# Kernel optimization log

Measured on AMD Instinct MI355X. Metric: run time of the kernel, lower is better.

## Reference

```python
import jax, jax.numpy as jnp
import numpy as np

Q_DIM = 1024
K_DIM = 1024
EMBED_DIM = 1024
NUM_HEADS = 16
HEAD_DIM = EMBED_DIM // NUM_HEADS
CLAMP = 50000.0
MASK_FILL = -9000000000000000.0


def _xavier(key, out_f, in_f):
    bound = float(np.sqrt(6.0 / (in_f + out_f)))
    return jax.random.uniform(key, (out_f, in_f), jnp.float32, -bound, bound)


def setup_inputs() -> dict:
    key = jax.random.key(0)
    ks = jax.random.split(key, 8)
    b, t, s = 2, 2048, 2048
    return {
        "q": jax.random.normal(ks[0], (b, t, Q_DIM), jnp.float32),
        "k": jax.random.normal(ks[1], (b, s, K_DIM), jnp.float32),
        "v": jax.random.normal(ks[2], (b, s, K_DIM), jnp.float32),
        "attention_mask": jax.random.randint(ks[3], (b, s), 0, 2, jnp.int32),
        "Wq": _xavier(ks[4], EMBED_DIM, Q_DIM), "bq": jnp.zeros((EMBED_DIM,), jnp.float32),
        "Wk": _xavier(ks[5], EMBED_DIM, K_DIM), "bk": jnp.zeros((EMBED_DIM,), jnp.float32),
        "Wv": _xavier(ks[6], EMBED_DIM, K_DIM), "bv": jnp.zeros((EMBED_DIM,), jnp.float32),
        "Wo": _xavier(ks[7], Q_DIM, EMBED_DIM), "bo": jnp.zeros((Q_DIM,), jnp.float32),
    }


def reference(q, k, v, attention_mask, Wq, bq, Wk, bk, Wv, bv, Wo, bo):
    b, t, _ = q.shape
    s = k.shape[1]
    scale = HEAD_DIM ** (-0.5)
    # projections, split heads: [b, h, len, d]
    qs = ((q @ Wq.T + bq) * scale).reshape(b, t, NUM_HEADS, HEAD_DIM).transpose(0, 2, 1, 3)
    ks = (k @ Wk.T + bk).reshape(b, s, NUM_HEADS, HEAD_DIM).transpose(0, 2, 1, 3)
    vs = (v @ Wv.T + bv).reshape(b, s, NUM_HEADS, HEAD_DIM).transpose(0, 2, 1, 3)
    # scores [b, h, t, s], clamp for under/overflow as in original
    attn = jnp.einsum("bhtd,bhsd->bhts", qs, ks)
    attn = jnp.clip(attn, -CLAMP, CLAMP)
    # 2D mask -> additive: zeros become -9e15, nonzeros are ADDED as-is (faithful to masked_fill semantics)
    m = attention_mask.astype(jnp.float32)
    m = jnp.where(m == 0, MASK_FILL, m)  # [b, s]
    attn = attn + m[:, None, None, :]
    attn = jax.nn.softmax(attn, axis=-1)
    # dropout p=0 / eval mode: identity
    out = jnp.einsum("bhts,bhsd->bthd", attn, vs).reshape(b, t, EMBED_DIM)
    out = out @ Wo.T + bo
    return out, attn.reshape(b * NUM_HEADS, t, s)
```

## Files before the change

kernel.cpp:

```cpp
#include <hip/hip_runtime.h>
#include <hip/hip_bf16.h>


typedef __attribute__((ext_vector_type(8))) __bf16 bf16x8;
typedef __attribute__((ext_vector_type(4))) float f32x4;
typedef __attribute__((ext_vector_type(8))) unsigned short us8;

#define MFMA16(A, B, C) __builtin_amdgcn_mfma_f32_16x16x32_bf16(A, B, C, 0, 0, 0)

__device__ __forceinline__ unsigned short f2bf(float f) {
  __bf16 h = (__bf16)f;
  return __builtin_bit_cast(unsigned short, h);
}

__global__ __launch_bounds__(256) void cvt_all_kernel(
    const float* __restrict__ q, const float* __restrict__ k, const float* __restrict__ v,
    const float* __restrict__ Wq, const float* __restrict__ Wk,
    const float* __restrict__ Wv, const float* __restrict__ Wo,
    unsigned short* __restrict__ qb, unsigned short* __restrict__ kb,
    unsigned short* __restrict__ vb, unsigned short* __restrict__ wqb,
    unsigned short* __restrict__ wkb, unsigned short* __restrict__ wvb,
    unsigned short* __restrict__ wob) {
  const int bid = blockIdx.x;
  const float* src;
  unsigned short* dst;
  int i;
  if (bid < 4096)       { src = q; dst = qb; i = bid * 256 + threadIdx.x; }
  else if (bid < 8192)  { src = k; dst = kb; i = (bid - 4096) * 256 + threadIdx.x; }
  else if (bid < 12288) { src = v; dst = vb; i = (bid - 8192) * 256 + threadIdx.x; }
  else {
    int wsel = (bid - 12288) >> 10;
    i = ((bid - 12288) & 1023) * 256 + threadIdx.x;
    src = wsel == 0 ? Wq : wsel == 1 ? Wk : wsel == 2 ? Wv : Wo;
    dst = wsel == 0 ? wqb : wsel == 1 ? wkb : wsel == 2 ? wvb : wob;
  }
  float4 vv = ((const float4*)src)[i];
  ushort4 o;
  o.x = f2bf(vv.x); o.y = f2bf(vv.y); o.z = f2bf(vv.z); o.w = f2bf(vv.w);
  ((ushort4*)dst)[i] = o;
}

template <bool OUT_F32>
__device__ __forceinline__ void gemm_body(
    const unsigned short* __restrict__ A, const unsigned short* __restrict__ Bw,
    const float* __restrict__ bias, void* __restrict__ Cout, float scale,
    int m0, int n0) {
  __shared__ short As[128 * 72];
  __shared__ short Bs[128 * 72];
  const int tid = threadIdx.x;
  const int l = tid & 63, w = tid >> 6;
  const int lq = l >> 4, lr = l & 15;
  const int wr = w >> 1, wc = w & 1;

  uint4 va[4], vb[4];
#pragma unroll
  for (int i = 0; i < 4; ++i) {
    int c = i * 256 + tid, r = c >> 3, c8 = c & 7;
    va[i] = *(const uint4*)(A + (size_t)(m0 + r) * 1024 + c8 * 8);
    vb[i] = *(const uint4*)(Bw + (size_t)(n0 + r) * 1024 + c8 * 8);
  }
  const f32x4 fz = {0.f, 0.f, 0.f, 0.f};
  f32x4 acc[4][4];
#pragma unroll
  for (int m = 0; m < 4; ++m)
#pragma unroll
    for (int n = 0; n < 4; ++n) acc[m][n] = fz;

  for (int ks = 0; ks < 16; ++ks) {
    __syncthreads();
#pragma unroll
    for (int i = 0; i < 4; ++i) {
      int c = i * 256 + tid, r = c >> 3, c8 = c & 7;
      *(uint4*)((char*)As + r * 144 + c8 * 16) = va[i];
      *(uint4*)((char*)Bs + r * 144 + c8 * 16) = vb[i];
    }
    __syncthreads();
    if (ks < 15) {
      int k0 = (ks + 1) * 64;
#pragma unroll
      for (int i = 0; i < 4; ++i) {
        int c = i * 256 + tid, r = c >> 3, c8 = c & 7;
        va[i] = *(const uint4*)(A + (size_t)(m0 + r) * 1024 + k0 + c8 * 8);
        vb[i] = *(const uint4*)(Bw + (size_t)(n0 + r) * 1024 + k0 + c8 * 8);
      }
    }
#pragma unroll
    for (int kk = 0; kk < 2; ++kk) {
      bf16x8 af[4], bfr[4];
#pragma unroll
      for (int m = 0; m < 4; ++m)
        af[m] = *(const bf16x8*)((const char*)As + (wr * 64 + m * 16 + lr) * 144 + kk * 64 + lq * 16);
#pragma unroll
      for (int n = 0; n < 4; ++n)
        bfr[n] = *(const bf16x8*)((const char*)Bs + (wc * 64 + n * 16 + lr) * 144 + kk * 64 + lq * 16);
#pragma unroll
      for (int m = 0; m < 4; ++m)
#pragma unroll
        for (int n = 0; n < 4; ++n) acc[m][n] = MFMA16(af[m], bfr[n], acc[m][n]);
    }
  }
#pragma unroll
  for (int n = 0; n < 4; ++n) {
    const int col = n0 + wc * 64 + n * 16 + lr;
    const float bv_ = bias[col];
#pragma unroll
    for (int m = 0; m < 4; ++m) {
      const int rowb = m0 + wr * 64 + m * 16 + lq * 4;
#pragma unroll
      for (int r = 0; r < 4; ++r) {
        float vv = (acc[m][n][r] + bv_) * scale;
        if (OUT_F32)
          ((float*)Cout)[(size_t)(rowb + r) * 1024 + col] = vv;
        else
          ((unsigned short*)Cout)[(size_t)(rowb + r) * 1024 + col] = f2bf(vv);
      }
    }
  }
}

__global__ __launch_bounds__(256) void gemm_qkv_kernel(
    const unsigned short* __restrict__ qb, const unsigned short* __restrict__ kb,
    const unsigned short* __restrict__ vb,
    const unsigned short* __restrict__ wqb, const unsigned short* __restrict__ wkb,
    const unsigned short* __restrict__ wvb,
    const float* __restrict__ bq, const float* __restrict__ bk, const float* __restrict__ bv,
    unsigned short* __restrict__ Qp, unsigned short* __restrict__ Kp,
    unsigned short* __restrict__ Vp) {
  const int z = blockIdx.z;
  const unsigned short* A = z == 0 ? qb : z == 1 ? kb : vb;
  const unsigned short* W = z == 0 ? wqb : z == 1 ? wkb : wvb;
  const float* bias = z == 0 ? bq : z == 1 ? bk : bv;
  unsigned short* C = z == 0 ? Qp : z == 1 ? Kp : Vp;
  const float scale = z == 0 ? 0.125f : 1.0f;
  gemm_body<false>(A, W, bias, C, scale, blockIdx.x * 128, blockIdx.y * 128);
}

__global__ __launch_bounds__(256) void gemm_o_kernel(
    const unsigned short* __restrict__ A, const unsigned short* __restrict__ Bw,
    const float* __restrict__ bias, float* __restrict__ Cout) {
  gemm_body<true>(A, Bw, bias, Cout, 1.0f, blockIdx.x * 128, blockIdx.y * 128);
}

__global__ __launch_bounds__(256) void transpose_v_kernel(const unsigned short* __restrict__ Vp,
                                                          unsigned short* __restrict__ Vt) {
  __shared__ unsigned short Ts[64 * 72];
  const int tid = threadIdx.x;
  const int kt = blockIdx.x;
  const int rt = blockIdx.y;
  const int b_ = rt >> 4, h_ = rt & 15;
#pragma unroll
  for (int i = 0; i < 2; ++i) {
    int c = i * 256 + tid, r = c >> 3, c8 = c & 7;
    uint4 v = *(const uint4*)(Vp + (size_t)(b_ * 2048 + kt * 64 + r) * 1024 + h_ * 64 + c8 * 8);
    *(uint4*)((char*)Ts + r * 144 + c8 * 16) = v;
  }
  __syncthreads();
#pragma unroll
  for (int i = 0; i < 2; ++i) {
    int c = i * 256 + tid, dr = c >> 3, k8 = c & 7;
    us8 t8;
#pragma unroll
    for (int j = 0; j < 8; ++j) t8[j] = Ts[(k8 * 8 + j) * 72 + dr];
    *(us8*)(Vt + (size_t)(rt * 64 + dr) * 2048 + kt * 64 + k8 * 8) = t8;
  }
}

__device__ __forceinline__ int pf_idx(int row, int col) {
  return row * 64 + (((col >> 2) ^ (row & 7)) << 2) + (col & 3);
}

__global__ __launch_bounds__(256) void attn_kernel(
    const unsigned short* __restrict__ Qp,
    const unsigned short* __restrict__ Kp,
    const unsigned short* __restrict__ Vt,
    const int* __restrict__ mask,
    float* __restrict__ attn_out,
    unsigned short* __restrict__ Obuf)
{
  __shared__ char smem[61440];
  short* Qs = (short*)smem;
  float* maskadd = (float*)(smem + 53248);

  const int tid = threadIdx.x;
  const int l = tid & 63, w = tid >> 6;
  const int lq = l >> 4, lr = l & 15;
  float* Pw = (float*)(smem + w * 4096);

  const int tb = blockIdx.x, h = blockIdx.y, bz = blockIdx.z;
  const size_t qrow0 = (size_t)bz * 2048 + tb * 64;
  const size_t krow0 = (size_t)bz * 2048;
  const size_t vrow0 = (size_t)(bz * 16 + h) * 64;

  for (int j = tid; j < 2048; j += 256) {
    int mv = mask[bz * 2048 + j];
    maskadd[j] = (mv == 0) ? -9.0e15f : (float)mv;
  }
#pragma unroll
  for (int i = 0; i < 2; ++i) {
    int c = i * 256 + tid, r = c >> 3, c8 = c & 7;
    uint4 v = *(const uint4*)(Qp + (qrow0 + r) * 1024 + h * 64 + c8 * 8);
    *(uint4*)((char*)Qs + r * 144 + c8 * 16) = v;
  }
  __syncthreads();
  bf16x8 aq[2];
#pragma unroll
  for (int kk = 0; kk < 2; ++kk)
    aq[kk] = *(const bf16x8*)((const char*)Qs + (w * 16 + lr) * 144 + kk * 64 + lq * 16);
  __syncthreads();

  const int r0 = tid >> 3, c8s = tid & 7;

#define KLOAD(d, kcv)                                                                       \
  {                                                                                         \
    d[0] = *(const uint4*)(Kp + (krow0 + (kcv)*64 + r0) * 1024 + h * 64 + c8s * 8);         \
    d[1] = *(const uint4*)(Kp + (krow0 + (kcv)*64 + 32 + r0) * 1024 + h * 64 + c8s * 8);    \
  }
#define VLOAD(d, kcv)                                                                       \
  {                                                                                         \
    d[0] = *(const uint4*)(Vt + (vrow0 + r0) * 2048 + (kcv)*64 + c8s * 8);                  \
    d[1] = *(const uint4*)(Vt + (vrow0 + 32 + r0) * 2048 + (kcv)*64 + c8s * 8);             \
  }
#define KWRITE(s, buf)                                                          \
  {                                                                             \
    *(uint4*)(smem + 16384 + (buf)*9216 + r0 * 144 + c8s * 16) = s[0];          \
    *(uint4*)(smem + 16384 + (buf)*9216 + (32 + r0) * 144 + c8s * 16) = s[1];   \
  }
#define VWRITE(s, buf)                                                          \
  {                                                                             \
    *(uint4*)(smem + 34816 + (buf)*9216 + r0 * 144 + c8s * 16) = s[0];          \
    *(uint4*)(smem + 34816 + (buf)*9216 + (32 + r0) * 144 + c8s * 16) = s[1];   \
  }
#define KFRAG(jt, kk) \
  (*(const bf16x8*)(smem + 16384 + (kc & 1) * 9216 + ((jt)*16 + lr) * 144 + (kk)*64 + lq * 16))
#define VFRAG(dt, kk) \
  (*(const bf16x8*)(smem + 34816 + (kc & 1) * 9216 + ((dt)*16 + lr) * 144 + (kk)*64 + lq * 16))

  float lacc[4] = {0.f, 0.f, 0.f, 0.f};
  {
    uint4 kr[2];
    KLOAD(kr, 0);
    KWRITE(kr, 0);
    __syncthreads();
    for (int kc = 0; kc < 32; ++kc) {
      uint4 kn[2];
      if (kc < 31) KLOAD(kn, kc + 1);
#pragma unroll
      for (int jt = 0; jt < 4; ++jt) {
        f32x4 sa = {0.f, 0.f, 0.f, 0.f};
        sa = MFMA16(aq[0], KFRAG(jt, 0), sa);
        sa = MFMA16(aq[1], KFRAG(jt, 1), sa);
        float ma = maskadd[kc * 64 + jt * 16 + lr];
#pragma unroll
        for (int r = 0; r < 4; ++r) {
          float s_ = fminf(fmaxf(sa[r], -50000.f), 50000.f) + ma;
          lacc[r] += __expf(s_);
        }
      }
      if (kc < 31) KWRITE(kn, (kc + 1) & 1);
      __syncthreads();
    }
  }
#pragma unroll
  for (int r = 0; r < 4; ++r) {
    float t = lacc[r];
    t += __shfl_xor(t, 1, 64);
    t += __shfl_xor(t, 2, 64);
    t += __shfl_xor(t, 4, 64);
    t += __shfl_xor(t, 8, 64);
    lacc[r] = 1.0f / t;
  }

  const f32x4 fz = {0.f, 0.f, 0.f, 0.f};
  f32x4 oacc[4];
#pragma unroll
  for (int dt = 0; dt < 4; ++dt) oacc[dt] = fz;
  const size_t arow = (size_t)(bz * 16 + h) * 2048 + tb * 64 + w * 16;

  {
    uint4 kr[2], vr[2];
    KLOAD(kr, 0);
    VLOAD(vr, 0);
    KWRITE(kr, 0);
    VWRITE(vr, 0);
    __syncthreads();
    for (int kc = 0; kc < 32; ++kc) {
      uint4 kn[2], vn[2];
      if (kc < 31) {
        KLOAD(kn, kc + 1);
        VLOAD(vn, kc + 1);
      }
#pragma unroll
      for (int jt = 0; jt < 4; ++jt) {
        f32x4 sa = {0.f, 0.f, 0.f, 0.f};
        sa = MFMA16(aq[0], KFRAG(jt, 0), sa);
        sa = MFMA16(aq[1], KFRAG(jt, 1), sa);
        float ma = maskadd[kc * 64 + jt * 16 + lr];
#pragma unroll
        for (int r = 0; r < 4; ++r) {
          float s_ = fminf(fmaxf(sa[r], -50000.f), 50000.f) + ma;
          Pw[pf_idx(lq * 4 + r, jt * 16 + lr)] = __expf(s_) * lacc[r];
        }
      }
#pragma unroll
      for (int it = 0; it < 4; ++it) {
        int row = it * 4 + lq;
        f32x4 pv4 = *(const f32x4*)&Pw[pf_idx(row, lr * 4)];
        f32x4* dst = (f32x4*)&attn_out[(arow + row) * 2048 + kc * 64 + lr * 4];
        __builtin_nontemporal_store(pv4, dst);
      }
#pragma unroll
      for (int kk = 0; kk < 2; ++kk) {
        f32x4 a0 = *(const f32x4*)&Pw[pf_idx(lr, kk * 32 + lq * 8)];
        f32x4 a1 = *(const f32x4*)&Pw[pf_idx(lr, kk * 32 + lq * 8 + 4)];
        bf16x8 ap;
#pragma unroll
        for (int j = 0; j < 4; ++j) {
          ap[j] = (__bf16)a0[j];
          ap[4 + j] = (__bf16)a1[j];
        }
#pragma unroll
        for (int dt = 0; dt < 4; ++dt)
          oacc[dt] = MFMA16(ap, VFRAG(dt, kk), oacc[dt]);
      }
      if (kc < 31) {
        KWRITE(kn, (kc + 1) & 1);
        VWRITE(vn, (kc + 1) & 1);
      }
      __syncthreads();
    }
  }
#pragma unroll
  for (int dt = 0; dt < 4; ++dt) {
    int col = h * 64 + dt * 16 + lr;
#pragma unroll
    for (int r = 0; r < 4; ++r) {
      int trow = tb * 64 + w * 16 + lq * 4 + r;
      Obuf[((size_t)bz * 2048 + trow) * 1024 + col] = f2bf(oacc[dt][r]);
    }
  }
#undef KLOAD
#undef VLOAD
#undef KWRITE
#undef VWRITE
#undef KFRAG
#undef VFRAG
}

extern "C" void kernel_launch(void* const* d_in, const int* in_sizes, int n_in,
                              void* d_out, int out_size, void* d_ws, size_t ws_size,
                              hipStream_t stream) {
  (void)in_sizes; (void)n_in; (void)out_size; (void)ws_size;
  const float* q  = (const float*)d_in[0];
  const float* k  = (const float*)d_in[1];
  const float* v  = (const float*)d_in[2];
  const int* msk  = (const int*)d_in[3];
  const float* Wq = (const float*)d_in[4];
  const float* bq = (const float*)d_in[5];
  const float* Wk = (const float*)d_in[6];
  const float* bk = (const float*)d_in[7];
  const float* Wv = (const float*)d_in[8];
  const float* bv = (const float*)d_in[9];
  const float* Wo = (const float*)d_in[10];
  const float* bo = (const float*)d_in[11];

  unsigned short* p = (unsigned short*)d_ws;
  unsigned short* qb  = p; p += 4194304;
  unsigned short* kb  = p; p += 4194304;
  unsigned short* vb  = p; p += 4194304;
  unsigned short* wqb = p; p += 1048576;
  unsigned short* wkb = p; p += 1048576;
  unsigned short* wvb = p; p += 1048576;
  unsigned short* wob = p; p += 1048576;
  unsigned short* Qp  = p; p += 4194304;
  unsigned short* Kp  = p; p += 4194304;
  unsigned short* Vp  = p; p += 4194304;
  unsigned short* Vtg = p; p += 4194304;
  unsigned short* Ob  = p; p += 4194304;

  cvt_all_kernel<<<16384, 256, 0, stream>>>(q, k, v, Wq, Wk, Wv, Wo,
                                            qb, kb, vb, wqb, wkb, wvb, wob);

  gemm_qkv_kernel<<<dim3(32, 8, 3), 256, 0, stream>>>(qb, kb, vb, wqb, wkb, wvb,
                                                      bq, bk, bv, Qp, Kp, Vp);

  transpose_v_kernel<<<dim3(32, 32), 256, 0, stream>>>(Vp, Vtg);

  float* outp = (float*)d_out;
  float* attnp = outp + 4194304;
  attn_kernel<<<dim3(32, 16, 2), 256, 0, stream>>>(Qp, Kp, Vtg, msk, attnp, Ob);

  gemm_o_kernel<<<dim3(32, 8), 256, 0, stream>>>(Ob, wob, bo, outp);
}
```

Baseline: 332.9 us.

## Fuse fp32-to-bf16 conversion into GEMM loads and precompute additive mask

Result: slower. 414.5 us (+24.5%).

```diff
diff --git a/kernel.cpp b/kernel.cpp
--- a/kernel.cpp
+++ b/kernel.cpp
@@ -12,37 +12,22 @@
   __bf16 h = (__bf16)f;
   return __builtin_bit_cast(unsigned short, h);
 }
-
-__global__ __launch_bounds__(256) void cvt_all_kernel(
-    const float* __restrict__ q, const float* __restrict__ k, const float* __restrict__ v,
-    const float* __restrict__ Wq, const float* __restrict__ Wk,
-    const float* __restrict__ Wv, const float* __restrict__ Wo,
-    unsigned short* __restrict__ qb, unsigned short* __restrict__ kb,
-    unsigned short* __restrict__ vb, unsigned short* __restrict__ wqb,
-    unsigned short* __restrict__ wkb, unsigned short* __restrict__ wvb,
-    unsigned short* __restrict__ wob) {
-  const int bid = blockIdx.x;
-  const float* src;
-  unsigned short* dst;
-  int i;
-  if (bid < 4096)       { src = q; dst = qb; i = bid * 256 + threadIdx.x; }
-  else if (bid < 8192)  { src = k; dst = kb; i = (bid - 4096) * 256 + threadIdx.x; }
-  else if (bid < 12288) { src = v; dst = vb; i = (bid - 8192) * 256 + threadIdx.x; }
-  else {
-    int wsel = (bid - 12288) >> 10;
-    i = ((bid - 12288) & 1023) * 256 + threadIdx.x;
-    src = wsel == 0 ? Wq : wsel == 1 ? Wk : wsel == 2 ? Wv : Wo;
-    dst = wsel == 0 ? wqb : wsel == 1 ? wkb : wsel == 2 ? wvb : wob;
-  }
-  float4 vv = ((const float4*)src)[i];
-  ushort4 o;
-  o.x = f2bf(vv.x); o.y = f2bf(vv.y); o.z = f2bf(vv.z); o.w = f2bf(vv.w);
-  ((ushort4*)dst)[i] = o;
-}
-
-template <bool OUT_F32>
+__device__ __forceinline__ ushort4 f4tob4(float4 f) {
+  ushort4 t;
+  t.x = f2bf(f.x); t.y = f2bf(f.y); t.z = f2bf(f.z); t.w = f2bf(f.w);
+  return t;
+}
+
+__global__ __launch_bounds__(256) void mask_cvt_kernel(const int* __restrict__ msk,
+                                                       float* __restrict__ maskf) {
+  int i = blockIdx.x * 256 + threadIdx.x;
+  int mv = msk[i];
+  maskf[i] = (mv == 0) ? -9.0e15f : (float)mv;
+}
+
+template <bool A_F32, bool OUT_F32>
 __device__ __forceinline__ void gemm_body(
-    const unsigned short* __restrict__ A, const unsigned short* __restrict__ Bw,
+    const void* __restrict__ Ap, const float* __restrict__ Bw,
     const float* __restrict__ bias, void* __restrict__ Cout, float scale,
     int m0, int n0) {
   __shared__ short As[128 * 72];
@@ -52,13 +37,59 @@
   const int lq = l >> 4, lr = l & 15;
   const int wr = w >> 1, wc = w & 1;
 
-  uint4 va[4], vb[4];
-#pragma unroll
-  for (int i = 0; i < 4; ++i) {
-    int c = i * 256 + tid, r = c >> 3, c8 = c & 7;
-    va[i] = *(const uint4*)(A + (size_t)(m0 + r) * 1024 + c8 * 8);
-    vb[i] = *(const uint4*)(Bw + (size_t)(n0 + r) * 1024 + c8 * 8);
-  }
+  ushort4 va8[8];
+  uint4 va4[4];
+  ushort4 vb8[8];
+
+#define LOAD_A(k0)                                                                 \
+  {                                                                                \
+    if (A_F32) {                                                                   \
+      const float* Af = (const float*)Ap;                                          \
+      _Pragma("unroll") for (int i = 0; i < 8; ++i) {                              \
+        int c = i * 256 + tid, r = c >> 4, c4 = c & 15;                            \
+        float4 f = *(const float4*)(Af + (size_t)(m0 + r) * 1024 + (k0) + c4 * 4); \
+        va8[i] = f4tob4(f);                                                        \
+      }                                                                            \
+    } else {                                                                       \
+      const unsigned short* Ab = (const unsigned short*)Ap;                        \
+      _Pragma("unroll") for (int i = 0; i < 4; ++i) {                              \
+        int c = i * 256 + tid, r = c >> 3, c8 = c & 7;                             \
+        va4[i] = *(const uint4*)(Ab + (size_t)(m0 + r) * 1024 + (k0) + c8 * 8);    \
+      }                                                                            \
+    }                                                                              \
+  }
+#define LOAD_B(k0)                                                                 \
+  {                                                                                \
+    _Pragma("unroll") for (int i = 0; i < 8; ++i) {                                \
+      int c = i * 256 + tid, r = c >> 4, c4 = c & 15;                              \
+      float4 f = *(const float4*)(Bw + (size_t)(n0 + r) * 1024 + (k0) + c4 * 4);   \
+      vb8[i] = f4tob4(f);                                                          \
+    }                                                                              \
+  }
+#define WRITE_A()                                                    \
+  {                                                                  \
+    if (A_F32) {                                                     \
+      _Pragma("unroll") for (int i = 0; i < 8; ++i) {                \
+        int c = i * 256 + tid, r = c >> 4, c4 = c & 15;              \
+        *(ushort4*)((char*)As + r * 144 + c4 * 8) = va8[i];          \
+      }                                                              \
+    } else {                                                         \
+      _Pragma("unroll") for (int i = 0; i < 4; ++i) {                \
+        int c = i * 256 + tid, r = c >> 3, c8 = c & 7;               \
+        *(uint4*)((char*)As + r * 144 + c8 * 16) = va4[i];           \
+      }                                                              \
+    }                                                                \
+  }
+#define WRITE_B()                                                    \
+  {                                                                  \
+    _Pragma("unroll") for (int i = 0; i < 8; ++i) {                  \
+      int c = i * 256 + tid, r = c >> 4, c4 = c & 15;                \
+      *(ushort4*)((char*)Bs + r * 144 + c4 * 8) = vb8[i];            \
+    }                                                                \
+  }
+
+  LOAD_A(0);
+  LOAD_B(0);
   const f32x4 fz = {0.f, 0.f, 0.f, 0.f};
   f32x4 acc[4][4];
 #pragma unroll
@@ -68,21 +99,13 @@
 
   for (int ks = 0; ks < 16; ++ks) {
     __syncthreads();
-#pragma unroll
-    for (int i = 0; i < 4; ++i) {
-      int c = i * 256 + tid, r = c >> 3, c8 = c & 7;
-      *(uint4*)((char*)As + r * 144 + c8 * 16) = va[i];
-      *(uint4*)((char*)Bs + r * 144 + c8 * 16) = vb[i];
-    }
+    WRITE_A();
+    WRITE_B();
     __syncthreads();
     if (ks < 15) {
       int k0 = (ks + 1) * 64;
-#pragma unroll
-      for (int i = 0; i < 4; ++i) {
-        int c = i * 256 + tid, r = c >> 3, c8 = c & 7;
-        va[i] = *(const uint4*)(A + (size_t)(m0 + r) * 1024 + k0 + c8 * 8);
-        vb[i] = *(const uint4*)(Bw + (size_t)(n0 + r) * 1024 + k0 + c8 * 8);
-      }
+      LOAD_A(k0);
+      LOAD_B(k0);
     }
 #pragma unroll
     for (int kk = 0; kk < 2; ++kk) {
@@ -116,29 +139,31 @@
       }
     }
   }
+#undef LOAD_A
+#undef LOAD_B
+#undef WRITE_A
+#undef WRITE_B
 }
 
 __global__ __launch_bounds__(256) void gemm_qkv_kernel(
-    const unsigned short* __restrict__ qb, const unsigned short* __restrict__ kb,
-    const unsigned short* __restrict__ vb,
-    const unsigned short* __restrict__ wqb, const unsigned short* __restrict__ wkb,
-    const unsigned short* __restrict__ wvb,
+    const float* __restrict__ q, const float* __restrict__ k, const float* __restrict__ v,
+    const float* __restrict__ Wq, const float* __restrict__ Wk, const float* __restrict__ Wv,
     const float* __restrict__ bq, const float* __restrict__ bk, const float* __restrict__ bv,
     unsigned short* __restrict__ Qp, unsigned short* __restrict__ Kp,
     unsigned short* __restrict__ Vp) {
   const int z = blockIdx.z;
-  const unsigned short* A = z == 0 ? qb : z == 1 ? kb : vb;
-  const unsigned short* W = z == 0 ? wqb : z == 1 ? wkb : wvb;
+  const float* A = z == 0 ? q : z == 1 ? k : v;
+  const float* W = z == 0 ? Wq : z == 1 ? Wk : Wv;
   const float* bias = z == 0 ? bq : z == 1 ? bk : bv;
   unsigned short* C = z == 0 ? Qp : z == 1 ? Kp : Vp;
   const float scale = z == 0 ? 0.125f : 1.0f;
-  gemm_body<false>(A, W, bias, C, scale, blockIdx.x * 128, blockIdx.y * 128);
+  gemm_body<true, false>(A, W, bias, C, scale, blockIdx.x * 128, blockIdx.y * 128);
 }
 
 __global__ __launch_bounds__(256) void gemm_o_kernel(
-    const unsigned short* __restrict__ A, const unsigned short* __restrict__ Bw,
+    const unsigned short* __restrict__ A, const float* __restrict__ Wo,
     const float* __restrict__ bias, float* __restrict__ Cout) {
-  gemm_body<true>(A, Bw, bias, Cout, 1.0f, blockIdx.x * 128, blockIdx.y * 128);
+  gemm_body<false, true>(A, Wo, bias, Cout, 1.0f, blockIdx.x * 128, blockIdx.y * 128);
 }
 
 __global__ __launch_bounds__(256) void transpose_v_kernel(const unsigned short* __restrict__ Vp,
@@ -173,13 +198,12 @@
     const unsigned short* __restrict__ Qp,
     const unsigned short* __restrict__ Kp,
     const unsigned short* __restrict__ Vt,
-    const int* __restrict__ mask,
+    const float* __restrict__ maskf,
     float* __restrict__ attn_out,
     unsigned short* __restrict__ Obuf)
 {
-  __shared__ char smem[61440];
+  __shared__ char smem[53248];
   short* Qs = (short*)smem;
-  float* maskadd = (float*)(smem + 53248);
 
   const int tid = threadIdx.x;
   const int l = tid & 63, w = tid >> 6;
@@ -190,11 +214,8 @@
   const size_t qrow0 = (size_t)bz * 2048 + tb * 64;
   const size_t krow0 = (size_t)bz * 2048;
   const size_t vrow0 = (size_t)(bz * 16 + h) * 64;
-
-  for (int j = tid; j < 2048; j += 256) {
-    int mv = mask[bz * 2048 + j];
-    maskadd[j] = (mv == 0) ? -9.0e15f : (float)mv;
-  }
+  const float* mrow = maskf + bz * 2048;
+
 #pragma unroll
   for (int i = 0; i < 2; ++i) {
     int c = i * 256 + tid, r = c >> 3, c8 = c & 7;
@@ -249,7 +270,7 @@
         f32x4 sa = {0.f, 0.f, 0.f, 0.f};
         sa = MFMA16(aq[0], KFRAG(jt, 0), sa);
         sa = MFMA16(aq[1], KFRAG(jt, 1), sa);
-        float ma = maskadd[kc * 64 + jt * 16 + lr];
+        float ma = mrow[kc * 64 + jt * 16 + lr];
 #pragma unroll
         for (int r = 0; r < 4; ++r) {
           float s_ = fminf(fmaxf(sa[r], -50000.f), 50000.f) + ma;
@@ -294,7 +315,7 @@
         f32x4 sa = {0.f, 0.f, 0.f, 0.f};
         sa = MFMA16(aq[0], KFRAG(jt, 0), sa);
         sa = MFMA16(aq[1], KFRAG(jt, 1), sa);
-        float ma = maskadd[kc * 64 + jt * 16 + lr];
+        float ma = mrow[kc * 64 + jt * 16 + lr];
 #pragma unroll
         for (int r = 0; r < 4; ++r) {
           float s_ = fminf(fmaxf(sa[r], -50000.f), 50000.f) + ma;
@@ -364,30 +385,23 @@
   const float* bo = (const float*)d_in[11];
 
   unsigned short* p = (unsigned short*)d_ws;
-  unsigned short* qb  = p; p += 4194304;
-  unsigned short* kb  = p; p += 4194304;
-  unsigned short* vb  = p; p += 4194304;
-  unsigned short* wqb = p; p += 1048576;
-  unsigned short* wkb = p; p += 1048576;
-  unsigned short* wvb = p; p += 1048576;
-  unsigned short* wob = p; p += 1048576;
   unsigned short* Qp  = p; p += 4194304;
   unsigned short* Kp  = p; p += 4194304;
   unsigned short* Vp  = p; p += 4194304;
   unsigned short* Vtg = p; p += 4194304;
   unsigned short* Ob  = p; p += 4194304;
-
-  cvt_all_kernel<<<16384, 256, 0, stream>>>(q, k, v, Wq, Wk, Wv, Wo,
-                                            qb, kb, vb, wqb, wkb, wvb, wob);
-
-  gemm_qkv_kernel<<<dim3(32, 8, 3), 256, 0, stream>>>(qb, kb, vb, wqb, wkb, wvb,
+  float* maskf = (float*)p;
+
+  mask_cvt_kernel<<<16, 256, 0, stream>>>(msk, maskf);
+
+  gemm_qkv_kernel<<<dim3(32, 8, 3), 256, 0, stream>>>(q, k, v, Wq, Wk, Wv,
                                                       bq, bk, bv, Qp, Kp, Vp);
 
   transpose_v_kernel<<<dim3(32, 32), 256, 0, stream>>>(Vp, Vtg);
 
   float* outp = (float*)d_out;
   float* attnp = outp + 4194304;
-  attn_kernel<<<dim3(32, 16, 2), 256, 0, stream>>>(Qp, Kp, Vtg, msk, attnp, Ob);
-
-  gemm_o_kernel<<<dim3(32, 8), 256, 0, stream>>>(Ob, wob, bo, outp);
-}
+  attn_kernel<<<dim3(32, 16, 2), 256, 0, stream>>>(Qp, Kp, Vtg, maskf, attnp, Ob);
+
+  gemm_o_kernel<<<dim3(32, 8), 256, 0, stream>>>(Ob, Wo, bo, outp);
+}
```

## Split attention into separate denominator pass and probability/output pass kernels

Applied to the files above, without the earlier changes.

Measured after the change: 353.0 us. +6.1%, slower.

```diff
diff --git a/kernel.cpp b/kernel.cpp
--- a/kernel.cpp
+++ b/kernel.cpp
@@ -169,27 +169,19 @@
   return row * 64 + (((col >> 2) ^ (row & 7)) << 2) + (col & 3);
 }
 
-__global__ __launch_bounds__(256) void attn_kernel(
-    const unsigned short* __restrict__ Qp,
-    const unsigned short* __restrict__ Kp,
-    const unsigned short* __restrict__ Vt,
-    const int* __restrict__ mask,
-    float* __restrict__ attn_out,
-    unsigned short* __restrict__ Obuf)
-{
-  __shared__ char smem[61440];
+__global__ __launch_bounds__(256) void attn_passA_kernel(
+    const unsigned short* __restrict__ Qp, const unsigned short* __restrict__ Kp,
+    const int* __restrict__ mask, float* __restrict__ denom) {
+  __shared__ char smem[26624];
   short* Qs = (short*)smem;
-  float* maskadd = (float*)(smem + 53248);
+  float* maskadd = (float*)(smem + 18432);
 
   const int tid = threadIdx.x;
   const int l = tid & 63, w = tid >> 6;
   const int lq = l >> 4, lr = l & 15;
-  float* Pw = (float*)(smem + w * 4096);
-
   const int tb = blockIdx.x, h = blockIdx.y, bz = blockIdx.z;
   const size_t qrow0 = (size_t)bz * 2048 + tb * 64;
   const size_t krow0 = (size_t)bz * 2048;
-  const size_t vrow0 = (size_t)(bz * 16 + h) * 64;
 
   for (int j = tid; j < 2048; j += 256) {
     int mv = mask[bz * 2048 + j];
@@ -210,45 +202,33 @@
 
   const int r0 = tid >> 3, c8s = tid & 7;
 
-#define KLOAD(d, kcv)                                                                       \
+#define KLOADA(d, kcv)                                                                      \
   {                                                                                         \
     d[0] = *(const uint4*)(Kp + (krow0 + (kcv)*64 + r0) * 1024 + h * 64 + c8s * 8);         \
     d[1] = *(const uint4*)(Kp + (krow0 + (kcv)*64 + 32 + r0) * 1024 + h * 64 + c8s * 8);    \
   }
-#define VLOAD(d, kcv)                                                                       \
-  {                                                                                         \
-    d[0] = *(const uint4*)(Vt + (vrow0 + r0) * 2048 + (kcv)*64 + c8s * 8);                  \
-    d[1] = *(const uint4*)(Vt + (vrow0 + 32 + r0) * 2048 + (kcv)*64 + c8s * 8);             \
-  }
-#define KWRITE(s, buf)                                                          \
-  {                                                                             \
-    *(uint4*)(smem + 16384 + (buf)*9216 + r0 * 144 + c8s * 16) = s[0];          \
-    *(uint4*)(smem + 16384 + (buf)*9216 + (32 + r0) * 144 + c8s * 16) = s[1];   \
-  }
-#define VWRITE(s, buf)                                                          \
-  {                                                                             \
-    *(uint4*)(smem + 34816 + (buf)*9216 + r0 * 144 + c8s * 16) = s[0];          \
-    *(uint4*)(smem + 34816 + (buf)*9216 + (32 + r0) * 144 + c8s * 16) = s[1];   \
-  }
-#define KFRAG(jt, kk) \
-  (*(const bf16x8*)(smem + 16384 + (kc & 1) * 9216 + ((jt)*16 + lr) * 144 + (kk)*64 + lq * 16))
-#define VFRAG(dt, kk) \
-  (*(const bf16x8*)(smem + 34816 + (kc & 1) * 9216 + ((dt)*16 + lr) * 144 + (kk)*64 + lq * 16))
+#define KWRITEA(s, buf)                                                 \
+  {                                                                     \
+    *(uint4*)(smem + (buf)*9216 + r0 * 144 + c8s * 16) = s[0];          \
+    *(uint4*)(smem + (buf)*9216 + (32 + r0) * 144 + c8s * 16) = s[1];   \
+  }
+#define KFRAGA(jt, kk) \
+  (*(const bf16x8*)(smem + (kc & 1) * 9216 + ((jt)*16 + lr) * 144 + (kk)*64 + lq * 16))
 
   float lacc[4] = {0.f, 0.f, 0.f, 0.f};
   {
     uint4 kr[2];
-    KLOAD(kr, 0);
-    KWRITE(kr, 0);
+    KLOADA(kr, 0);
+    KWRITEA(kr, 0);
     __syncthreads();
     for (int kc = 0; kc < 32; ++kc) {
       uint4 kn[2];
-      if (kc < 31) KLOAD(kn, kc + 1);
+      if (kc < 31) KLOADA(kn, kc + 1);
 #pragma unroll
       for (int jt = 0; jt < 4; ++jt) {
         f32x4 sa = {0.f, 0.f, 0.f, 0.f};
-        sa = MFMA16(aq[0], KFRAG(jt, 0), sa);
-        sa = MFMA16(aq[1], KFRAG(jt, 1), sa);
+        sa = MFMA16(aq[0], KFRAGA(jt, 0), sa);
+        sa = MFMA16(aq[1], KFRAGA(jt, 1), sa);
         float ma = maskadd[kc * 64 + jt * 16 + lr];
 #pragma unroll
         for (int r = 0; r < 4; ++r) {
@@ -256,7 +236,7 @@
           lacc[r] += __expf(s_);
         }
       }
-      if (kc < 31) KWRITE(kn, (kc + 1) & 1);
+      if (kc < 31) KWRITEA(kn, (kc + 1) & 1);
       __syncthreads();
     }
   }
@@ -267,8 +247,85 @@
     t += __shfl_xor(t, 2, 64);
     t += __shfl_xor(t, 4, 64);
     t += __shfl_xor(t, 8, 64);
-    lacc[r] = 1.0f / t;
-  }
+    lacc[r] = t;
+  }
+  if (lr == 0) {
+#pragma unroll
+    for (int r = 0; r < 4; ++r)
+      denom[((size_t)bz * 16 + h) * 2048 + tb * 64 + w * 16 + lq * 4 + r] = lacc[r];
+  }
+#undef KLOADA
+#undef KWRITEA
+#undef KFRAGA
+}
+
+__global__ __launch_bounds__(256) void attn_passB_kernel(
+    const unsigned short* __restrict__ Qp, const unsigned short* __restrict__ Kp,
+    const unsigned short* __restrict__ Vt, const int* __restrict__ mask,
+    const float* __restrict__ denom, float* __restrict__ attn_out,
+    unsigned short* __restrict__ Obuf) {
+  __shared__ char smem[61440];
+  short* Qs = (short*)smem;
+  float* maskadd = (float*)(smem + 53248);
+
+  const int tid = threadIdx.x;
+  const int l = tid & 63, w = tid >> 6;
+  const int lq = l >> 4, lr = l & 15;
+  float* Pw = (float*)(smem + w * 4096);
+
+  const int tb = blockIdx.x, h = blockIdx.y, bz = blockIdx.z;
+  const size_t qrow0 = (size_t)bz * 2048 + tb * 64;
+  const size_t krow0 = (size_t)bz * 2048;
+  const size_t vrow0 = (size_t)(bz * 16 + h) * 64;
+
+  for (int j = tid; j < 2048; j += 256) {
+    int mv = mask[bz * 2048 + j];
+    maskadd[j] = (mv == 0) ? -9.0e15f : (float)mv;
+  }
+#pragma unroll
+  for (int i = 0; i < 2; ++i) {
+    int c = i * 256 + tid, r = c >> 3, c8 = c & 7;
+    uint4 v = *(const uint4*)(Qp + (qrow0 + r) * 1024 + h * 64 + c8 * 8);
+    *(uint4*)((char*)Qs + r * 144 + c8 * 16) = v;
+  }
+  __syncthreads();
+  bf16x8 aq[2];
+#pragma unroll
+  for (int kk = 0; kk < 2; ++kk)
+    aq[kk] = *(const bf16x8*)((const char*)Qs + (w * 16 + lr) * 144 + kk * 64 + lq * 16);
+  __syncthreads();
+
+  float lacc[4];
+#pragma unroll
+  for (int r = 0; r < 4; ++r)
+    lacc[r] = 1.0f / denom[((size_t)bz * 16 + h) * 2048 + tb * 64 + w * 16 + lq * 4 + r];
+
+  const int r0 = tid >> 3, c8s = tid & 7;
+
+#define KLOAD(d, kcv)                                                                       \
+  {                                                                                         \
+    d[0] = *(const uint4*)(Kp + (krow0 + (kcv)*64 + r0) * 1024 + h * 64 + c8s * 8);         \
+    d[1] = *(const uint4*)(Kp + (krow0 + (kcv)*64 + 32 + r0) * 1024 + h * 64 + c8s * 8);    \
+  }
+#define VLOAD(d, kcv)                                                                       \
+  {                                                                                         \
+    d[0] = *(const uint4*)(Vt + (vrow0 + r0) * 2048 + (kcv)*64 + c8s * 8);                  \
+    d[1] = *(const uint4*)(Vt + (vrow0 + 32 + r0) * 2048 + (kcv)*64 + c8s * 8);             \
+  }
+#define KWRITE(s, buf)                                                          \
+  {                                                                             \
+    *(uint4*)(smem + 16384 + (buf)*9216 + r0 * 144 + c8s * 16) = s[0];          \
+    *(uint4*)(smem + 16384 + (buf)*9216 + (32 + r0) * 144 + c8s * 16) = s[1];   \
+  }
+#define VWRITE(s, buf)                                                          \
+  {                                                                             \
+    *(uint4*)(smem + 34816 + (buf)*9216 + r0 * 144 + c8s * 16) = s[0];          \
+    *(uint4*)(smem + 34816 + (buf)*9216 + (32 + r0) * 144 + c8s * 16) = s[1];   \
+  }
+#define KFRAG(jt, kk) \
+  (*(const bf16x8*)(smem + 16384 + (kc & 1) * 9216 + ((jt)*16 + lr) * 144 + (kk)*64 + lq * 16))
+#define VFRAG(dt, kk) \
+  (*(const bf16x8*)(smem + 34816 + (kc & 1) * 9216 + ((dt)*16 + lr) * 144 + (kk)*64 + lq * 16))
 
   const f32x4 fz = {0.f, 0.f, 0.f, 0.f};
   f32x4 oacc[4];
@@ -376,6 +433,7 @@
   unsigned short* Vp  = p; p += 4194304;
   unsigned short* Vtg = p; p += 4194304;
   unsigned short* Ob  = p; p += 4194304;
+  float* denom = (float*)p;
 
   cvt_all_kernel<<<16384, 256, 0, stream>>>(q, k, v, Wq, Wk, Wv, Wo,
                                             qb, kb, vb, wqb, wkb, wvb, wob);
@@ -387,7 +445,10 @@
 
   float* outp = (float*)d_out;
   float* attnp = outp + 4194304;
-  attn_kernel<<<dim3(32, 16, 2), 256, 0, stream>>>(Qp, Kp, Vtg, msk, attnp, Ob);
+
+  attn_passA_kernel<<<dim3(32, 16, 2), 256, 0, stream>>>(Qp, Kp, msk, denom);
+  attn_passB_kernel<<<dim3(32, 16, 2), 256, 0, stream>>>(Qp, Kp, Vtg, msk, denom,
+                                                         attnp, Ob);
 
   gemm_o_kernel<<<dim3(32, 8), 256, 0, stream>>>(Ob, wob, bo, outp);
 }
```
